# Kernel optimization log

Measured on AMD Instinct MI355X. Metric: run time of the kernel, lower is better.

## Reference

```python
import jax, jax.numpy as jnp
import numpy as np

TOP_K = 10
RANKING_WEIGHT = 0.3
UP_WEIGHT = 1.0
DOWN_WEIGHT = 0.5
NEG = 1e9  # finite stand-in for -inf so softmax/grads stay NaN-free


def setup_inputs() -> dict:
    key = jax.random.key(0)
    k1, k2, k3, k4 = jax.random.split(key, 4)
    B, N = 1024, 5000
    up_logits = jax.random.normal(k1, (B, N), jnp.float32)
    down_logits = jax.random.normal(k2, (B, N), jnp.float32)
    y_true = jax.random.normal(k3, (B, N), jnp.float32) * 0.05  # daily returns
    masks = jax.random.randint(k4, (B, N), 0, 2).astype(jnp.int32)
    return {"up_logits": up_logits, "down_logits": down_logits,
            "y_true": y_true, "masks": masks}


def _bce_with_logits(x, z):
    # softplus(x) - x*z  ==  -[z*log(sig(x)) + (1-z)*log(1-sig(x))]
    return jax.nn.softplus(x) - x * z


def reference(up_logits, down_logits, y_true, masks):
    maskb = masks > 0                                   # [B, N]
    maskf = maskb.astype(up_logits.dtype)
    num_valid = maskf.sum(-1)                           # [B]
    nv_safe = jnp.maximum(num_valid, 1.0)
    k = jnp.minimum(TOP_K, num_valid.astype(jnp.int32))  # [B] min(top_k, num)

    # Descending rank of y_true among valid entries (invalid pushed to bottom).
    y_desc = jnp.where(maskb, y_true, -NEG)
    rank_desc = jnp.argsort(jnp.argsort(-y_desc, axis=-1), axis=-1)  # [B, N]
    up_labels = (rank_desc < k[:, None]).astype(up_logits.dtype)

    # Ascending rank (biggest losers) for down path.
    y_asc = jnp.where(maskb, y_true, NEG)
    rank_asc = jnp.argsort(jnp.argsort(y_asc, axis=-1), axis=-1)
    down_labels = (rank_asc < k[:, None]).astype(down_logits.dtype)

    # Mean BCE over valid entries per row.
    up_loss = jnp.sum(_bce_with_logits(up_logits, up_labels) * maskf, -1) / nv_safe
    down_loss = jnp.sum(_bce_with_logits(down_logits, down_labels) * maskf, -1) / nv_safe

    # Listwise KL: softmax over valid entries; kl_div(log p, q, 'batchmean')
    # with 1D input of size num divides the sum by num.
    logp = jax.nn.log_softmax(jnp.where(maskb, up_logits, -NEG), axis=-1)
    logq = jax.nn.log_softmax(jnp.where(maskb, y_true, -NEG), axis=-1)
    q = jnp.exp(logq)
    kl = jnp.sum(jnp.where(maskb, q * (logq - logp), 0.0), -1) / nv_safe

    batch_loss = UP_WEIGHT * up_loss + DOWN_WEIGHT * down_loss + RANKING_WEIGHT * kl
    batch_loss = jnp.where(num_valid > 0, batch_loss, 0.0)  # skip empty rows
    return jnp.sum(batch_loss) / up_logits.shape[0]
```

## Files before the change

kernel.cpp:

```cpp
#include <hip/hip_runtime.h>
#include <math.h>

#define NCOLS 5000
#define NF4   1250
#define QBLK  4
#define QF4   313
#define BLOCK 256
#define NWAVES (BLOCK / 64)
#define TOPKK 10
#define TR    3
#define CAP   64


__device__ __forceinline__ unsigned mono_f32(float f) {
  unsigned u = __float_as_uint(f);
  return (u & 0x80000000u) ? ~u : (u | 0x80000000u);
}

__device__ __forceinline__ float wave_sum_f(float v) {
#pragma unroll
  for (int o = 1; o < 64; o <<= 1) v += __shfl_xor(v, o);
  return v;
}
__device__ __forceinline__ int wave_sum_i(int v) {
#pragma unroll
  for (int o = 1; o < 64; o <<= 1) v += __shfl_xor(v, o);
  return v;
}
__device__ __forceinline__ unsigned wave_max_u(unsigned v) {
#pragma unroll
  for (int o = 1; o < 64; o <<= 1) {
    unsigned w = __shfl_xor(v, o);
    v = w > v ? w : v;
  }
  return v;
}

extern "C" __global__ __launch_bounds__(BLOCK, 6)
void part_kernel(const float* __restrict__ up, const float* __restrict__ down,
                 const float* __restrict__ yt, const int* __restrict__ masks,
                 float* __restrict__ ws_sums, float2* __restrict__ ws_top,
                 float2* __restrict__ ws_bot) {
  __shared__ float red_f[7][NWAVES];
  __shared__ unsigned t1w_t[NWAVES], t1w_b[NWAVES];
  __shared__ unsigned keys_t[CAP]; __shared__ float vals_t[CAP];
  __shared__ unsigned keys_b[CAP]; __shared__ float vals_b[CAP];
  __shared__ int ct, cb;

  const int tid = threadIdx.x;
  const int lane = tid & 63;
  const int wv = tid >> 6;
  const int bq = blockIdx.x;
  const int row = bq >> 2;
  const int q = bq & 3;
  const int s = q * QF4;
  const int e = (s + QF4) < NF4 ? (s + QF4) : NF4;
  const int cnt = e - s;
  const long long b4 = (long long)row * NF4 + s;

  if (tid == 0) { ct = 0; cb = 0; }
  if (tid < CAP) {
    keys_t[tid] = 0u; vals_t[tid] = 0.f;
    keys_b[tid] = 0u; vals_b[tid] = 0.f;
  }

  const float4* up4 = (const float4*)up + b4;
  const float4* dn4 = (const float4*)down + b4;
  const float4* yt4 = (const float4*)yt + b4;
  const int4*   mk4 = (const int4*)masks + b4;

  const int t2 = BLOCK + tid;
  const bool inb2 = t2 < cnt;
  const int f2 = inb2 ? t2 : cnt - 1;
  float4 y0 = yt4[tid], u0 = up4[tid], d0 = dn4[tid];
  float4 y1 = yt4[f2],  u1 = up4[f2],  d1 = dn4[f2];
  int4   m0 = mk4[tid], m1 = mk4[f2];
  __builtin_amdgcn_sched_barrier(0);

  int nv_l = 0;
  float sq = 0.f, sp = 0.f, seyy = 0.f, seyu = 0.f, aspu = 0.f, aspd = 0.f;
  unsigned kk[8]; float ua[8], da[8];
  unsigned tmax = 0u, tbmax = 0u;

#define ELEM(idx, Y, U, D, M, INB)                                      \
  {                                                                     \
    const bool valid = (INB) && ((M) > 0);                              \
    const float y = (Y), u = (U), d = (D);                              \
    const unsigned kd = valid ? mono_f32(y) : 0u;                       \
    const unsigned kb = valid ? ~kd : 0u;                               \
    kk[idx] = kd; ua[idx] = u; da[idx] = d;                             \
    tmax = kd > tmax ? kd : tmax;                                       \
    tbmax = kb > tbmax ? kb : tbmax;                                    \
    if (valid) {                                                        \
      nv_l++;                                                           \
      const float ey = __expf(y);                                       \
      const float eu = __expf(u);                                       \
      const float ed = __expf(d);                                       \
      sq += ey; seyy += ey * y; seyu += ey * u; sp += eu;               \
      aspu += (u > 15.f) ? u : __logf(1.f + eu);                        \
      aspd += (d > 15.f) ? d : __logf(1.f + ed);                        \
    }                                                                   \
  }

  ELEM(0, y0.x, u0.x, d0.x, m0.x, true)
  ELEM(1, y0.y, u0.y, d0.y, m0.y, true)
  ELEM(2, y0.z, u0.z, d0.z, m0.z, true)
  ELEM(3, y0.w, u0.w, d0.w, m0.w, true)
  ELEM(4, y1.x, u1.x, d1.x, m1.x, inb2)
  ELEM(5, y1.y, u1.y, d1.y, m1.y, inb2)
  ELEM(6, y1.z, u1.z, d1.z, m1.z, inb2)
  ELEM(7, y1.w, u1.w, d1.w, m1.w, inb2)
#undef ELEM

  nv_l = wave_sum_i(nv_l);
  sq = wave_sum_f(sq);
  sp = wave_sum_f(sp);
  seyy = wave_sum_f(seyy);
  seyu = wave_sum_f(seyu);
  aspu = wave_sum_f(aspu);
  aspd = wave_sum_f(aspd);
  if (lane == 0) {
    red_f[0][wv] = (float)nv_l;
    red_f[1][wv] = sq;  red_f[2][wv] = sp;
    red_f[3][wv] = seyy; red_f[4][wv] = seyu;
    red_f[5][wv] = aspu; red_f[6][wv] = aspd;
  }

  {
    unsigned vt = tmax, vb = tbmax, t1t = 0u, t1b = 0u;
#pragma unroll
    for (int r = 0; r < TR; ++r) {
      unsigned mt = wave_max_u(vt);
      unsigned mb = wave_max_u(vb);
      if (vt == mt) vt = 0u;
      if (vb == mb) vb = 0u;
      t1t = mt; t1b = mb;
    }
    if (lane == 0) { t1w_t[wv] = t1t; t1w_b[wv] = t1b; }
  }
  __syncthreads();

  unsigned tq_t = 0xFFFFFFFFu, tq_b = 0xFFFFFFFFu;
#pragma unroll
  for (int w = 0; w < NWAVES; ++w) {
    tq_t = t1w_t[w] < tq_t ? t1w_t[w] : tq_t;
    tq_b = t1w_b[w] < tq_b ? t1w_b[w] : tq_b;
  }

  if (tid < 7) {
    float sm = red_f[tid][0] + red_f[tid][1] + red_f[tid][2] + red_f[tid][3];
    ws_sums[bq * 8 + tid] = sm;
  }

#pragma unroll
  for (int i = 0; i < 8; ++i) {
    const unsigned kd = kk[i];
    if (kd != 0u) {
      if (kd >= tq_t) {
        int p = atomicAdd(&ct, 1);
        if (p < CAP) { keys_t[p] = kd; vals_t[p] = ua[i]; }
      }
      const unsigned kb = ~kd;
      if (kb >= tq_b) {
        int p = atomicAdd(&cb, 1);
        if (p < CAP) { keys_b[p] = kb; vals_b[p] = da[i]; }
      }
    }
  }
  __syncthreads();

  if (tid < CAP) {
    ws_top[bq * CAP + tid] = make_float2(__uint_as_float(keys_t[tid]), vals_t[tid]);
  } else if (tid < 2 * CAP) {
    const int i = tid - CAP;
    ws_bot[bq * CAP + i] = make_float2(__uint_as_float(keys_b[i]), vals_b[i]);
  }
}

extern "C" __global__ __launch_bounds__(256, 4)
void finish_kernel(const float* __restrict__ ws_sums,
                   const float2* __restrict__ ws_top,
                   const float2* __restrict__ ws_bot,
                   float* __restrict__ out, int nrows, float inv_nrows) {
  __shared__ float wl[NWAVES];
  const int tid = threadIdx.x;
  const int lane = tid & 63;
  const int wv = tid >> 6;
  const int row = blockIdx.x * NWAVES + wv;

  float loss = 0.f;
  if (row < nrows) {
    float v = 0.f;
    if (lane < 32) v = ws_sums[(row * QBLK + (lane >> 3)) * 8 + (lane & 7)];
    v += __shfl_xor(v, 8);
    v += __shfl_xor(v, 16);
    const float nvf = __shfl(v, 0);
    const int nv = (int)nvf;
    if (nv > 0) {
      const int k = nv < TOPKK ? nv : TOPKK;
      const int cb0 = row * QBLK * CAP;
      unsigned kt[4], kb[4]; float vt[4], vb[4];
#pragma unroll
      for (int t = 0; t < 4; ++t) {
        const float2 a = ws_top[cb0 + t * 64 + lane];
        const float2 b = ws_bot[cb0 + t * 64 + lane];
        kt[t] = __float_as_uint(a.x); vt[t] = a.y;
        kb[t] = __float_as_uint(b.x); vb[t] = b.y;
      }
      unsigned thr_t = 0u, thr_b = 0u;
#pragma unroll
      for (int b = 31; b >= 0; --b) {
        const unsigned tt = thr_t | (1u << b);
        const unsigned tb = thr_b | (1u << b);
        int c1 = 0, c2 = 0;
#pragma unroll
        for (int t = 0; t < 4; ++t) {
          c1 += __popcll(__ballot(kt[t] >= tt));
          c2 += __popcll(__ballot(kb[t] >= tb));
        }
        thr_t = (c1 >= k) ? tt : thr_t;
        thr_b = (c2 >= k) ? tb : thr_b;
      }
      float su = 0.f, sd = 0.f;
#pragma unroll
      for (int t = 0; t < 4; ++t) {
        if (kt[t] >= thr_t && kt[t] != 0u) su += vt[t];
        if (kb[t] >= thr_b && kb[t] != 0u) sd += vb[t];
      }
      su = wave_sum_f(su);
      sd = wave_sum_f(sd);
      const float SQ  = __shfl(v, 1), SP  = __shfl(v, 2);
      const float SYY = __shfl(v, 3), SYU = __shfl(v, 4);
      const float ASU = __shfl(v, 5), ASD = __shfl(v, 6);
      const float kl = (SYY - SYU) / SQ - __logf(SQ) + __logf(SP);
      loss = ((ASU - su) + 0.5f * (ASD - sd) + 0.3f * kl) / nvf;
    }
  }
  if (lane == 0) wl[wv] = loss;
  __syncthreads();
  if (tid == 0) {
    atomicAdd(out, (wl[0] + wl[1] + wl[2] + wl[3]) * inv_nrows);
  }
}

extern "C" void kernel_launch(void* const* d_in, const int* in_sizes, int n_in,
                              void* d_out, int out_size, void* d_ws, size_t ws_size,
                              hipStream_t stream) {
  const float* up_logits   = (const float*)d_in[0];
  const float* down_logits = (const float*)d_in[1];
  const float* y_true      = (const float*)d_in[2];
  const int*   masks       = (const int*)d_in[3];

  const int nrows = in_sizes[0] / NCOLS;
  const int nrq = nrows * QBLK;
  const size_t need = (size_t)nrq * (8 + 4 * CAP) * sizeof(float);

  hipMemsetAsync(d_out, 0, sizeof(float) * (size_t)out_size, stream);

  float* wsf = (float*)d_ws;
  float* ws_sums = wsf;
  float2* ws_top = (float2*)(wsf + (size_t)nrq * 8);
  float2* ws_bot = ws_top + (size_t)nrq * CAP;
  (void)need; (void)ws_size;

  part_kernel<<<nrq, BLOCK, 0, stream>>>(up_logits, down_logits, y_true, masks,
                                         ws_sums, ws_top, ws_bot);
  const int p2blocks = (nrows + NWAVES - 1) / NWAVES;
  finish_kernel<<<p2blocks, 256, 0, stream>>>(ws_sums, ws_top, ws_bot,
                                              (float*)d_out, nrows,
                                              1.0f / (float)nrows);
}
```

Before: 124.8 us.

## Stream inputs via global_load_lds, prune per-quarter candidates to top-16, product softplus

The y/up/down quarter-row tiles are loaded straight into LDS with global_load_lds, and wave 0 overlaps its two chunks using explicit vmcnt waits. Softplus sums become a running product of (1+e^x) followed by a single log, which removes per-element logs and branches. Each block now runs an in-block radix threshold select and writes only 16 candidates per quarter instead of 64, so the finish kernel handles one float2 per lane. Risks: the product of up to 8 terms can overflow for large logits (the u>15 guard is gone), exp is computed for invalid elements too, and the LDS staging may limit occupancy.

```diff
diff --git a/kernel.cpp b/kernel.cpp
--- a/kernel.cpp
+++ b/kernel.cpp
@@ -3,20 +3,19 @@
 
 #define NCOLS 5000
 #define NF4   1250
-#define QBLK  4
 #define QF4   313
 #define BLOCK 256
-#define NWAVES (BLOCK / 64)
+#define NWAVES 4
 #define TOPKK 10
 #define TR    3
 #define CAP   64
+#define OUTK  16
 
 
 __device__ __forceinline__ unsigned mono_f32(float f) {
   unsigned u = __float_as_uint(f);
   return (u & 0x80000000u) ? ~u : (u | 0x80000000u);
 }
-
 __device__ __forceinline__ float wave_sum_f(float v) {
 #pragma unroll
   for (int o = 1; o < 64; o <<= 1) v += __shfl_xor(v, o);
@@ -35,16 +34,22 @@
   }
   return v;
 }
-
-extern "C" __global__ __launch_bounds__(BLOCK, 6)
+__device__ __forceinline__ void gl_lds16(const float4* g, float4* l) {
+  __builtin_amdgcn_global_load_lds(
+      (const __attribute__((address_space(1))) void*)(g),
+      (__attribute__((address_space(3))) void*)(l), 16, 0, 0);
+}
+
+extern "C" __global__ __launch_bounds__(BLOCK, 8)
 void part_kernel(const float* __restrict__ up, const float* __restrict__ down,
                  const float* __restrict__ yt, const int* __restrict__ masks,
                  float* __restrict__ ws_sums, float2* __restrict__ ws_top,
                  float2* __restrict__ ws_bot) {
+  __shared__ float4 y_s[320], u_s[320], d_s[320];
   __shared__ float red_f[7][NWAVES];
   __shared__ unsigned t1w_t[NWAVES], t1w_b[NWAVES];
-  __shared__ unsigned keys_t[CAP]; __shared__ float vals_t[CAP];
-  __shared__ unsigned keys_b[CAP]; __shared__ float vals_b[CAP];
+  __shared__ unsigned keys_t[CAP]; __shared__ int col_t[CAP];
+  __shared__ unsigned keys_b[CAP]; __shared__ int col_b[CAP];
   __shared__ int ct, cb;
 
   const int tid = threadIdx.x;
@@ -53,131 +58,232 @@
   const int bq = blockIdx.x;
   const int row = bq >> 2;
   const int q = bq & 3;
-  const int s = q * QF4;
-  const int e = (s + QF4) < NF4 ? (s + QF4) : NF4;
-  const int cnt = e - s;
-  const long long b4 = (long long)row * NF4 + s;
+  const int qlen = (q == 3) ? (NF4 - 3 * QF4) : QF4;
+  const long long b4 = (long long)row * NF4 + q * QF4;
 
   if (tid == 0) { ct = 0; cb = 0; }
-  if (tid < CAP) {
-    keys_t[tid] = 0u; vals_t[tid] = 0.f;
-    keys_b[tid] = 0u; vals_b[tid] = 0.f;
-  }
-
-  const float4* up4 = (const float4*)up + b4;
-  const float4* dn4 = (const float4*)down + b4;
-  const float4* yt4 = (const float4*)yt + b4;
-  const int4*   mk4 = (const int4*)masks + b4;
-
-  const int t2 = BLOCK + tid;
-  const bool inb2 = t2 < cnt;
-  const int f2 = inb2 ? t2 : cnt - 1;
-  float4 y0 = yt4[tid], u0 = up4[tid], d0 = dn4[tid];
-  float4 y1 = yt4[f2],  u1 = up4[f2],  d1 = dn4[f2];
-  int4   m0 = mk4[tid], m1 = mk4[f2];
+
+  const float4* yt4q = (const float4*)yt + b4;
+  const float4* up4q = (const float4*)up + b4;
+  const float4* dn4q = (const float4*)down + b4;
+  const int4*   mk4q = (const int4*)masks + b4;
+
+  const int4 mA = mk4q[tid];
+  int4 mB = make_int4(0, 0, 0, 0);
+  if (wv == 0) mB = mk4q[(256 + tid < qlen) ? (256 + tid) : (qlen - 1)];
   __builtin_amdgcn_sched_barrier(0);
 
-  int nv_l = 0;
-  float sq = 0.f, sp = 0.f, seyy = 0.f, seyu = 0.f, aspu = 0.f, aspd = 0.f;
-  unsigned kk[8]; float ua[8], da[8];
+  {
+    const int wb = wv * 64;
+    gl_lds16(yt4q + wb + lane, y_s + wb);
+    gl_lds16(up4q + wb + lane, u_s + wb);
+    gl_lds16(dn4q + wb + lane, d_s + wb);
+    if (wv == 0) {
+      const int fB = (256 + lane < qlen) ? (256 + lane) : (qlen - 1);
+      gl_lds16(yt4q + fB, y_s + 256);
+      gl_lds16(up4q + fB, u_s + 256);
+      gl_lds16(dn4q + fB, d_s + 256);
+    }
+  }
+  __builtin_amdgcn_sched_barrier(0);
+
+  int vmask = 0;
+  float sq = 0.f, sp = 0.f, seyy = 0.f, seyu = 0.f;
+  float pu = 1.f, pd = 1.f;
   unsigned tmax = 0u, tbmax = 0u;
 
-#define ELEM(idx, Y, U, D, M, INB)                                      \
+#define ELEM(bit, Y, U, D, M, INB)                                      \
   {                                                                     \
     const bool valid = (INB) && ((M) > 0);                              \
     const float y = (Y), u = (U), d = (D);                              \
     const unsigned kd = valid ? mono_f32(y) : 0u;                       \
-    const unsigned kb = valid ? ~kd : 0u;                               \
-    kk[idx] = kd; ua[idx] = u; da[idx] = d;                             \
+    const unsigned kb2 = valid ? ~kd : 0u;                              \
+    vmask |= valid ? (1 << (bit)) : 0;                                  \
     tmax = kd > tmax ? kd : tmax;                                       \
-    tbmax = kb > tbmax ? kb : tbmax;                                    \
-    if (valid) {                                                        \
-      nv_l++;                                                           \
-      const float ey = __expf(y);                                       \
-      const float eu = __expf(u);                                       \
-      const float ed = __expf(d);                                       \
-      sq += ey; seyy += ey * y; seyu += ey * u; sp += eu;               \
-      aspu += (u > 15.f) ? u : __logf(1.f + eu);                        \
-      aspd += (d > 15.f) ? d : __logf(1.f + ed);                        \
-    }                                                                   \
-  }
-
-  ELEM(0, y0.x, u0.x, d0.x, m0.x, true)
-  ELEM(1, y0.y, u0.y, d0.y, m0.y, true)
-  ELEM(2, y0.z, u0.z, d0.z, m0.z, true)
-  ELEM(3, y0.w, u0.w, d0.w, m0.w, true)
-  ELEM(4, y1.x, u1.x, d1.x, m1.x, inb2)
-  ELEM(5, y1.y, u1.y, d1.y, m1.y, inb2)
-  ELEM(6, y1.z, u1.z, d1.z, m1.z, inb2)
-  ELEM(7, y1.w, u1.w, d1.w, m1.w, inb2)
+    tbmax = kb2 > tbmax ? kb2 : tbmax;                                  \
+    const float mf = valid ? 1.f : 0.f;                                 \
+    const float ey = __expf(y);                                         \
+    const float eu = __expf(u);                                         \
+    const float ed = __expf(d);                                         \
+    const float mey = mf * ey;                                          \
+    sq += mey;                                                          \
+    seyy = fmaf(mey, y, seyy);                                          \
+    seyu = fmaf(mey, u, seyu);                                          \
+    sp += mf * eu;                                                      \
+    pu *= valid ? (1.f + eu) : 1.f;                                     \
+    pd *= valid ? (1.f + ed) : 1.f;                                     \
+  }
+
+#define CHUNKA()                                                        \
+  {                                                                     \
+    const float4 yv = y_s[tid];                                         \
+    const float4 uv = u_s[tid];                                         \
+    const float4 dv = d_s[tid];                                         \
+    ELEM(0, yv.x, uv.x, dv.x, mA.x, true)                               \
+    ELEM(1, yv.y, uv.y, dv.y, mA.y, true)                               \
+    ELEM(2, yv.z, uv.z, dv.z, mA.z, true)                               \
+    ELEM(3, yv.w, uv.w, dv.w, mA.w, true)                               \
+  }
+#define CHUNKB()                                                        \
+  {                                                                     \
+    const bool inbB = (256 + tid) < qlen;                               \
+    const float4 yv = y_s[256 + tid];                                   \
+    const float4 uv = u_s[256 + tid];                                   \
+    const float4 dv = d_s[256 + tid];                                   \
+    ELEM(4, yv.x, uv.x, dv.x, mB.x, inbB)                               \
+    ELEM(5, yv.y, uv.y, dv.y, mB.y, inbB)                               \
+    ELEM(6, yv.z, uv.z, dv.z, mB.z, inbB)                               \
+    ELEM(7, yv.w, uv.w, dv.w, mB.w, inbB)                               \
+  }
+
+  if (wv == 0) {
+    asm volatile("s_waitcnt vmcnt(3)" ::: "memory");
+    __builtin_amdgcn_sched_barrier(0);
+    CHUNKA()
+    asm volatile("s_waitcnt vmcnt(0)" ::: "memory");
+    __builtin_amdgcn_sched_barrier(0);
+    CHUNKB()
+  } else {
+    asm volatile("s_waitcnt vmcnt(0)" ::: "memory");
+    __builtin_amdgcn_sched_barrier(0);
+    CHUNKA()
+  }
+#undef CHUNKA
+#undef CHUNKB
 #undef ELEM
 
-  nv_l = wave_sum_i(nv_l);
+  const float aspu = __logf(pu);
+  const float aspd = __logf(pd);
+
+  int nv_l = wave_sum_i(__popc((unsigned)vmask));
   sq = wave_sum_f(sq);
   sp = wave_sum_f(sp);
   seyy = wave_sum_f(seyy);
   seyu = wave_sum_f(seyu);
-  aspu = wave_sum_f(aspu);
-  aspd = wave_sum_f(aspd);
+  const float au = wave_sum_f(aspu);
+  const float ad = wave_sum_f(aspd);
+
+  unsigned t1t = 0u, t1b_ = 0u;
+  {
+    unsigned vt = tmax, vb = tbmax;
+#pragma unroll
+    for (int r = 0; r < TR; ++r) {
+      const unsigned mt = wave_max_u(vt);
+      const unsigned mb_ = wave_max_u(vb);
+      if (vt == mt) vt = 0u;
+      if (vb == mb_) vb = 0u;
+      t1t = mt; t1b_ = mb_;
+    }
+  }
   if (lane == 0) {
     red_f[0][wv] = (float)nv_l;
     red_f[1][wv] = sq;  red_f[2][wv] = sp;
     red_f[3][wv] = seyy; red_f[4][wv] = seyu;
-    red_f[5][wv] = aspu; red_f[6][wv] = aspd;
-  }
+    red_f[5][wv] = au;  red_f[6][wv] = ad;
+    t1w_t[wv] = t1t; t1w_b[wv] = t1b_;
+  }
+  __syncthreads();
+
+  unsigned t1 = t1w_t[0], t1b = t1w_b[0];
+#pragma unroll
+  for (int w = 1; w < NWAVES; ++w) {
+    t1 = t1w_t[w] < t1 ? t1w_t[w] : t1;
+    t1b = t1w_b[w] < t1b ? t1w_b[w] : t1b;
+  }
+  const int nv_q = (int)(red_f[0][0] + red_f[0][1] + red_f[0][2] + red_f[0][3]);
 
   {
-    unsigned vt = tmax, vb = tbmax, t1t = 0u, t1b = 0u;
-#pragma unroll
-    for (int r = 0; r < TR; ++r) {
-      unsigned mt = wave_max_u(vt);
-      unsigned mb = wave_max_u(vb);
-      if (vt == mt) vt = 0u;
-      if (vb == mb) vb = 0u;
-      t1t = mt; t1b = mb;
-    }
-    if (lane == 0) { t1w_t[wv] = t1t; t1w_b[wv] = t1b; }
+    const int mbA = vmask & 0xF;
+    if (mbA) {
+      const float4 yv = y_s[tid];
+      const float ya[4] = {yv.x, yv.y, yv.z, yv.w};
+#pragma unroll
+      for (int c = 0; c < 4; ++c) {
+        if ((mbA >> c) & 1) {
+          const unsigned kd = mono_f32(ya[c]);
+          if (kd >= t1) {
+            const int i = atomicAdd(&ct, 1);
+            if (i < CAP) { keys_t[i] = kd; col_t[i] = (tid << 2) + c; }
+          }
+          const unsigned kb2 = ~kd;
+          if (kb2 >= t1b) {
+            const int i = atomicAdd(&cb, 1);
+            if (i < CAP) { keys_b[i] = kb2; col_b[i] = (tid << 2) + c; }
+          }
+        }
+      }
+    }
+    const int mbB = (vmask >> 4) & 0xF;
+    if (mbB) {
+      const float4 yv = y_s[256 + tid];
+      const float ya[4] = {yv.x, yv.y, yv.z, yv.w};
+#pragma unroll
+      for (int c = 0; c < 4; ++c) {
+        if ((mbB >> c) & 1) {
+          const unsigned kd = mono_f32(ya[c]);
+          if (kd >= t1) {
+            const int i = atomicAdd(&ct, 1);
+            if (i < CAP) { keys_t[i] = kd; col_t[i] = ((256 + tid) << 2) + c; }
+          }
+          const unsigned kb2 = ~kd;
+          if (kb2 >= t1b) {
+            const int i = atomicAdd(&cb, 1);
+            if (i < CAP) { keys_b[i] = kb2; col_b[i] = ((256 + tid) << 2) + c; }
+          }
+        }
+      }
+    }
   }
   __syncthreads();
 
-  unsigned tq_t = 0xFFFFFFFFu, tq_b = 0xFFFFFFFFu;
-#pragma unroll
-  for (int w = 0; w < NWAVES; ++w) {
-    tq_t = t1w_t[w] < tq_t ? t1w_t[w] : tq_t;
-    tq_b = t1w_b[w] < tq_b ? t1w_b[w] : tq_b;
-  }
-
-  if (tid < 7) {
-    float sm = red_f[tid][0] + red_f[tid][1] + red_f[tid][2] + red_f[tid][3];
-    ws_sums[bq * 8 + tid] = sm;
-  }
-
-#pragma unroll
-  for (int i = 0; i < 8; ++i) {
-    const unsigned kd = kk[i];
-    if (kd != 0u) {
-      if (kd >= tq_t) {
-        int p = atomicAdd(&ct, 1);
-        if (p < CAP) { keys_t[p] = kd; vals_t[p] = ua[i]; }
-      }
-      const unsigned kb = ~kd;
-      if (kb >= tq_b) {
-        int p = atomicAdd(&cb, 1);
-        if (p < CAP) { keys_b[p] = kb; vals_b[p] = da[i]; }
-      }
-    }
-  }
-  __syncthreads();
-
-  if (tid < CAP) {
-    ws_top[bq * CAP + tid] = make_float2(__uint_as_float(keys_t[tid]), vals_t[tid]);
-  } else if (tid < 2 * CAP) {
-    const int i = tid - CAP;
-    ws_bot[bq * CAP + i] = make_float2(__uint_as_float(keys_b[i]), vals_b[i]);
-  }
-}
-
-extern "C" __global__ __launch_bounds__(256, 4)
+  const int kq = nv_q < TOPKK ? nv_q : TOPKK;
+  if (wv == 0) {
+    const int n = ct < CAP ? ct : CAP;
+    const unsigned kc = (lane < n) ? keys_t[lane] : 0u;
+    unsigned thr = 0u;
+#pragma unroll
+    for (int bb = 31; bb >= 0; --bb) {
+      const unsigned t = thr | (1u << bb);
+      thr = (__popcll(__ballot(kc >= t)) >= kq) ? t : thr;
+    }
+    const bool sel = (kc >= thr) && (kc != 0u);
+    const unsigned long long msk = __ballot(sel);
+    const int idx = __popcll(msk & ((1ull << lane) - 1ull));
+    if (sel && idx < OUTK)
+      ws_top[bq * OUTK + idx] =
+          make_float2(__uint_as_float(kc), ((const float*)u_s)[col_t[lane]]);
+    int cnt = __popcll(msk);
+    cnt = cnt < OUTK ? cnt : OUTK;
+    if (lane >= cnt && lane < OUTK)
+      ws_top[bq * OUTK + lane] = make_float2(0.f, 0.f);
+  } else if (wv == 1) {
+    const int n = cb < CAP ? cb : CAP;
+    const unsigned kc = (lane < n) ? keys_b[lane] : 0u;
+    unsigned thr = 0u;
+#pragma unroll
+    for (int bb = 31; bb >= 0; --bb) {
+      const unsigned t = thr | (1u << bb);
+      thr = (__popcll(__ballot(kc >= t)) >= kq) ? t : thr;
+    }
+    const bool sel = (kc >= thr) && (kc != 0u);
+    const unsigned long long msk = __ballot(sel);
+    const int idx = __popcll(msk & ((1ull << lane) - 1ull));
+    if (sel && idx < OUTK)
+      ws_bot[bq * OUTK + idx] =
+          make_float2(__uint_as_float(kc), ((const float*)d_s)[col_b[lane]]);
+    int cnt = __popcll(msk);
+    cnt = cnt < OUTK ? cnt : OUTK;
+    if (lane >= cnt && lane < OUTK)
+      ws_bot[bq * OUTK + lane] = make_float2(0.f, 0.f);
+  } else if (wv == 2 && lane < 8) {
+    const float s = (lane < 7)
+        ? red_f[lane][0] + red_f[lane][1] + red_f[lane][2] + red_f[lane][3]
+        : 0.f;
+    ws_sums[bq * 8 + lane] = s;
+  }
+}
+
+extern "C" __global__ __launch_bounds__(256, 8)
 void finish_kernel(const float* __restrict__ ws_sums,
                    const float2* __restrict__ ws_top,
                    const float2* __restrict__ ws_bot,
@@ -191,45 +297,28 @@
   float loss = 0.f;
   if (row < nrows) {
     float v = 0.f;
-    if (lane < 32) v = ws_sums[(row * QBLK + (lane >> 3)) * 8 + (lane & 7)];
+    if (lane < 32) v = ws_sums[(row * 4 + (lane >> 3)) * 8 + (lane & 7)];
     v += __shfl_xor(v, 8);
     v += __shfl_xor(v, 16);
     const float nvf = __shfl(v, 0);
     const int nv = (int)nvf;
     if (nv > 0) {
       const int k = nv < TOPKK ? nv : TOPKK;
-      const int cb0 = row * QBLK * CAP;
-      unsigned kt[4], kb[4]; float vt[4], vb[4];
-#pragma unroll
-      for (int t = 0; t < 4; ++t) {
-        const float2 a = ws_top[cb0 + t * 64 + lane];
-        const float2 b = ws_bot[cb0 + t * 64 + lane];
-        kt[t] = __float_as_uint(a.x); vt[t] = a.y;
-        kb[t] = __float_as_uint(b.x); vb[t] = b.y;
+      const float2 a = ws_top[row * 64 + lane];
+      const float2 bt = ws_bot[row * 64 + lane];
+      const unsigned kt = __float_as_uint(a.x);
+      const unsigned kb = __float_as_uint(bt.x);
+      unsigned thr_t = 0u, thr_b = 0u;
+#pragma unroll
+      for (int bb = 31; bb >= 0; --bb) {
+        const unsigned tt = thr_t | (1u << bb);
+        const unsigned tb = thr_b | (1u << bb);
+        thr_t = (__popcll(__ballot(kt >= tt)) >= k) ? tt : thr_t;
+        thr_b = (__popcll(__ballot(kb >= tb)) >= k) ? tb : thr_b;
       }
-      unsigned thr_t = 0u, thr_b = 0u;
-#pragma unroll
-      for (int b = 31; b >= 0; --b) {
-        const unsigned tt = thr_t | (1u << b);
-        const unsigned tb = thr_b | (1u << b);
-        int c1 = 0, c2 = 0;
-#pragma unroll
-        for (int t = 0; t < 4; ++t) {
-          c1 += __popcll(__ballot(kt[t] >= tt));
-          c2 += __popcll(__ballot(kb[t] >= tb));
-        }
-        thr_t = (c1 >= k) ? tt : thr_t;
-        thr_b = (c2 >= k) ? tb : thr_b;
-      }
-      float su = 0.f, sd = 0.f;
-#pragma unroll
-      for (int t = 0; t < 4; ++t) {
-        if (kt[t] >= thr_t && kt[t] != 0u) su += vt[t];
-        if (kb[t] >= thr_b && kb[t] != 0u) sd += vb[t];
-      }
-      su = wave_sum_f(su);
-      sd = wave_sum_f(sd);
-      const float SQ  = __shfl(v, 1), SP  = __shfl(v, 2);
+      const float su = wave_sum_f((kt >= thr_t && kt != 0u) ? a.y : 0.f);
+      const float sd = wave_sum_f((kb >= thr_b && kb != 0u) ? bt.y : 0.f);
+      const float SQ = __shfl(v, 1), SP = __shfl(v, 2);
       const float SYY = __shfl(v, 3), SYU = __shfl(v, 4);
       const float ASU = __shfl(v, 5), ASD = __shfl(v, 6);
       const float kl = (SYY - SYU) / SQ - __logf(SQ) + __logf(SP);
@@ -238,9 +327,8 @@
   }
   if (lane == 0) wl[wv] = loss;
   __syncthreads();
-  if (tid == 0) {
+  if (tid == 0)
     atomicAdd(out, (wl[0] + wl[1] + wl[2] + wl[3]) * inv_nrows);
-  }
 }
 
 extern "C" void kernel_launch(void* const* d_in, const int* in_sizes, int n_in,
@@ -252,21 +340,17 @@
   const int*   masks       = (const int*)d_in[3];
 
   const int nrows = in_sizes[0] / NCOLS;
-  const int nrq = nrows * QBLK;
-  const size_t need = (size_t)nrq * (8 + 4 * CAP) * sizeof(float);
-
-  hipMemsetAsync(d_out, 0, sizeof(float) * (size_t)out_size, stream);
+  const int nrq = nrows * 4;
 
   float* wsf = (float*)d_ws;
   float* ws_sums = wsf;
   float2* ws_top = (float2*)(wsf + (size_t)nrq * 8);
-  float2* ws_bot = ws_top + (size_t)nrq * CAP;
-  (void)need; (void)ws_size;
-
+  float2* ws_bot = ws_top + (size_t)nrq * OUTK;
+  (void)ws_size;
+
+  hipMemsetAsync(d_out, 0, sizeof(float) * (size_t)out_size, stream);
   part_kernel<<<nrq, BLOCK, 0, stream>>>(up_logits, down_logits, y_true, masks,
                                          ws_sums, ws_top, ws_bot);
-  const int p2blocks = (nrows + NWAVES - 1) / NWAVES;
-  finish_kernel<<<p2blocks, 256, 0, stream>>>(ws_sums, ws_top, ws_bot,
-                                              (float*)d_out, nrows,
-                                              1.0f / (float)nrows);
-}
+  finish_kernel<<<(nrows + NWAVES - 1) / NWAVES, 256, 0, stream>>>(
+      ws_sums, ws_top, ws_bot, (float*)d_out, nrows, 1.0f / (float)nrows);
+}
```

Measured after the change: 122.4 us. No clear change (-1.9%).
